# Performance work log

Measured on AMD Instinct MI355X. Metric: run time of the kernel, lower is better.

## Reference

```python
import jax, jax.numpy as jnp
import numpy as np

BETA1, BETA2, BETA3 = 0.9, 0.8, 0.9
DECAY1, INC1 = 0.05, 5.0
DECAY3, INC3 = 0.05, 5.0
LATENCY = 4.0
B_CONST = 0.15
LIF1_MIN, LIF1_MAX = 150.0, 400.0
LIF3_MIN, LIF3_MAX = 50.0, 200.0
A_P, A_M, TAU_P, TAU_M = 0.01, 0.01, 20.0, 20.0  # exponential STDP params (params1/2/3)


def stdp(dt):
    # exponential STDP curve: potentiate when post fires after pre (dt>=0), depress otherwise
    return jnp.where(dt >= 0, A_P * jnp.exp(-dt / TAU_P), -A_M * jnp.exp(dt / TAU_M))


def setup_inputs() -> dict:
    key = jax.random.key(0)
    k1, k2, k3, k4 = jax.random.split(key, 4)
    H, N, C = 8192, 4096, 128
    return {
        "image": jax.random.uniform(k1, (N,), jnp.float32),
        "W1": jax.random.uniform(k2, (H, N), jnp.float32),
        "W2": jax.random.uniform(k3, (N, H), jnp.float32),
        "W3": jax.random.uniform(k4, (C, N), jnp.float32),
        "thr1": 100.0 * jnp.ones((H,), jnp.float32),
        "thr2": 5.0 * jnp.ones((N,), jnp.float32),
        "thr3": 100.0 * jnp.ones((C,), jnp.float32),
        "time": 256,
        "pw": 8,
    }


def reference(image, W1, W2, W3, thr1, thr2, thr3, time, pw):
    N = image.shape[0]
    H = W1.shape[0]
    C = W3.shape[0]
    T = int(time)
    Tf = jnp.float32(T)

    img_t = Tf * image  # input spike times, [N]
    # rate -> pulse encoding: input_spikes[t, i] = 1 for t in [floor(img_t[i]), floor(img_t[i])+pw)
    t_axis = jnp.arange(T, dtype=jnp.float32)[:, None]          # [T,1]
    start = jnp.floor(img_t)[None, :]                            # [1,N]
    input_spikes = ((t_axis >= start) & (t_axis < start + pw)).astype(jnp.float32)  # [T,N]

    def wta(mem, th):
        # winner-take-all (snntorch inhibition=True): only argmax neuron may spike
        j = jnp.argmax(mem)
        fire = (mem[j] > th[j]).astype(mem.dtype)
        return fire * jax.nn.one_hot(j, mem.shape[0], dtype=mem.dtype)

    def step(carry, xs):
        mem1, mem2, mem3, th1, th3, r1, r2, r3, hid_act, out_act = carry
        x, t = xs
        # layer 1: Leaky LIF, inhibition, reset-to-zero
        mem1 = BETA1 * mem1 + jnp.dot(W1, x)
        spk1 = wta(mem1, th1)
        mem1 = mem1 * (1.0 - spk1)
        # layer 2: Leaky LIF, no inhibition, reset-by-subtract
        mem2 = BETA2 * mem2 + jnp.dot(W2, spk1)
        spk2 = (mem2 > thr2).astype(mem2.dtype)
        mem2 = mem2 - spk2 * thr2
        # layer 3 (clustering): Leaky LIF, inhibition, zeroed after any spike
        mem3 = BETA3 * mem3 + jnp.dot(W3, spk2)
        spk3 = wta(mem3, th3)
        mem3 = mem3 - spk3 * th3
        mem3 = jnp.where(jnp.sum(spk3) > 0, 0.0, mem3)
        # first-spike-time recon (recon stays at first nonzero spk*(t+1))
        r1 = jnp.where(r1 != 0, r1, spk1 * (t + 1.0))
        r2 = jnp.where(r2 != 0, r2, spk2 * (t + 1.0))
        r3 = jnp.where(r3 != 0, r3, spk3 * (t + 1.0))
        hid_act = hid_act + spk1
        out_act = out_act + spk2
        # adaptive thresholds: homeostatic decay + spike-triggered increase, clamped
        th1 = jnp.clip(th1 - DECAY1 + INC1 * spk1, LIF1_MIN, LIF1_MAX)
        th3 = jnp.clip(th3 - DECAY3 + INC3 * spk3, LIF3_MIN, LIF3_MAX)
        return (mem1, mem2, mem3, th1, th3, r1, r2, r3, hid_act, out_act), None

    z = jnp.zeros
    carry0 = (z(H), z(N), z(C), thr1, thr3, z(H), z(N), z(C), z(H), z(N))
    (mem1, mem2, mem3, th1, th3, r1, r2, r3, hid_act, out_act), _ = jax.lax.scan(
        step, carry0, (input_spikes, jnp.arange(T, dtype=jnp.float32)))

    # neurons that never spiked get time T
    r1 = jnp.where(r1 == 0, Tf, r1)
    r2 = jnp.where(r2 == 0, Tf, r2)
    r3 = jnp.where(r3 == 0, Tf, r3)

    # STDP weight updates (exponential), same structure as PresentImage
    hid_mask = (hid_act > 0).astype(jnp.float32)
    delta_t1 = (r1[:, None] - img_t[None, :]) * hid_mask[:, None]      # [H,N]
    W1_new = W1 + stdp(delta_t1)
    delta_t2 = r2[:, None] - r1[None, :]                                # [N,H]
    zeta = (Tf - r1) * hid_mask / Tf                                    # [H]
    rho = (r2 - LATENCY - img_t) / Tf + B_CONST                         # [N]
    W2_new = jnp.clip(W2 + stdp(delta_t2) * (rho[:, None] * zeta[None, :]), 0.0, 1.0)
    delta_t3 = r3[:, None] - r2[None, :]                                # [C,N]
    W3_new = W3 + stdp(delta_t3)

    error = (img_t - (r2 - LATENCY)) / Tf
    error_scalar = jnp.sum(jnp.square(error))
    return (error, error_scalar, r1, r2, r3, W1_new, W2_new, W3_new)
```

## Files before the change

### kernel.cpp

```cpp
#include <hip/hip_runtime.h>
#include <cstdint>
#include <cstddef>

#define Hn 8192
#define Nn 4096
#define Cn 128
#define Tt 256
#define CAP 192

typedef unsigned long long ull;

__device__ __forceinline__ float th_lazy2(float b, float lo, float hi, int nup){
    if (nup <= 0) return b;
    float a = fminf(fmaxf(__fsub_rn(b, 0.05f), lo), hi);
    if (nup == 1) return a;
    return fmaxf(__fsub_rn(a, __fmul_rn(0.05f, (float)(nup - 1))), lo);
}

__device__ __forceinline__ float clamp01(float v){
    return fminf(fmaxf(v, 0.f), 1.f);
}

template<int CTRL>
__device__ __forceinline__ int dpp_i(int x, int old){
    return __builtin_amdgcn_update_dpp(old, x, CTRL, 0xf, 0xf, false);
}
__device__ __forceinline__ float wave_max_f(float v){
    const int NEG = __float_as_int(-3.4e38f);
#define STEPM(C) { float o = __int_as_float(dpp_i<C>(__float_as_int(v), NEG)); v = fmaxf(v, o); }
    STEPM(0x111) STEPM(0x112) STEPM(0x114) STEPM(0x118) STEPM(0x142) STEPM(0x143)
#undef STEPM
    return __int_as_float(__builtin_amdgcn_readlane(__float_as_int(v), 63));
}
__device__ __forceinline__ int wave_argmax_l(float bv, int bh, float &wv, int &wh){
    float v = wave_max_f(bv);
    ull tie = __ballot(bv == v);
    int tl = __ffsll((long long)tie) - 1;
    int h = __builtin_amdgcn_readlane(bh, tl);
    if (__builtin_expect(__popcll(tie) > 1, 0)){
        ull m = tie & (tie - 1);
        while (m){
            int l2 = __ffsll((long long)m) - 1;
            int h2 = __builtin_amdgcn_readlane(bh, l2);
            if (h2 < h){ h = h2; tl = l2; }
            m &= m - 1;
        }
    }
    wv = v; wh = h; return tl;
}
__device__ __forceinline__ float rl_f(float x, int l){
    return __int_as_float(__builtin_amdgcn_readlane(__float_as_int(x), l));
}

__global__ __launch_bounds__(1024) void k_prep(const float* __restrict__ image,
        int* __restrict__ boff, int* __restrict__ sidx, unsigned* __restrict__ anyv){
    __shared__ int s_start[Nn];
    __shared__ int s_c4[4][Tt];
    __shared__ int s_boff[Tt + 1];
    int tid = threadIdx.x;
    for (int i = tid; i < Nn; i += 1024)
        s_start[i] = (int)floorf(__fmul_rn(256.f, image[i]));
    if (tid < Tt) anyv[tid] = 0u;
    __syncthreads();
    int b = tid & 255, q = tid >> 8;
    {
        int c = 0;
        for (int k = 0; k < 1024; ++k) c += (s_start[q * 1024 + k] == b) ? 1 : 0;
        s_c4[q][b] = c;
    }
    __syncthreads();
    if (tid == 0){
        int acc = 0;
        for (int bb = 0; bb < Tt; ++bb){
            s_boff[bb] = acc;
            acc += s_c4[0][bb] + s_c4[1][bb] + s_c4[2][bb] + s_c4[3][bb];
        }
        s_boff[Tt] = acc;
    }
    __syncthreads();
    if (tid <= Tt) boff[tid] = s_boff[tid];
    int p = s_boff[b];
    if (q > 0) p += s_c4[0][b];
    if (q > 1) p += s_c4[1][b];
    if (q > 2) p += s_c4[2][b];
    for (int k = 0; k < 1024; ++k){
        int i = q * 1024 + k;
        if (s_start[i] == b) sidx[p++] = i;
    }
}

__global__ __launch_bounds__(256) void k_gbuckets(const float* __restrict__ W1,
        const int* __restrict__ boff, const int* __restrict__ sidx,
        float* __restrict__ G_T){
    __shared__ float rows[4][Nn];
    int tid = threadIdx.x;
    int h0 = blockIdx.x * 4;
    for (int r = 0; r < 4; ++r){
        const float4* src = (const float4*)(W1 + (size_t)(h0 + r) * Nn);
        float4* dst = (float4*)rows[r];
        for (int j = tid; j < Nn / 4; j += 256) dst[j] = src[j];
    }
    __syncthreads();
    int t = tid;
    int b0 = boff[t], b1 = boff[t + 1];
    float s0 = 0.f, s1 = 0.f, s2 = 0.f, s3 = 0.f;
    for (int k = b0; k < b1; ++k){
        int i = sidx[k];
        s0 += rows[0][i]; s1 += rows[1][i]; s2 += rows[2][i]; s3 += rows[3][i];
    }
    G_T[(size_t)(h0 + 0) * Tt + t] = s0;
    G_T[(size_t)(h0 + 1) * Tt + t] = s1;
    G_T[(size_t)(h0 + 2) * Tt + t] = s2;
    G_T[(size_t)(h0 + 3) * Tt + t] = s3;
}

__global__ __launch_bounds__(256) void k_c1M(const float* __restrict__ G_T,
        float* __restrict__ M, float* __restrict__ r1pre, float* __restrict__ o_r1){
    __shared__ float tile[32][Tt + 1];
    __shared__ float c1s[32][Tt + 1];
    const int tid = threadIdx.x;
    const int h0 = blockIdx.x * 32;
    for (int r = 0; r < 32; ++r) tile[r][tid] = G_T[(size_t)(h0 + r) * Tt + tid];
    __syncthreads();
    {
        int hs = tid & 31, ts = tid >> 5;
        for (int tb = 0; tb < 32; ++tb){
            int t = tb * 8 + ts;
            int lo = (t - 7 < 0) ? 0 : t - 7;
            float s = 0.f;
            for (int u = lo; u <= t; ++u) s += tile[hs][u];
            c1s[hs][t] = s;
        }
    }
    __syncthreads();
    if (tid < 32){
        float m = 0.f;
        for (int t = 0; t < Tt; ++t){
            m = __fadd_rn(__fmul_rn(0.9f, m), c1s[tid][t]);
            M[(size_t)t * Hn + h0 + tid] = m;
        }
        r1pre[h0 + tid] = 0.f;
        o_r1[h0 + tid] = 256.f;
    }
}

__global__ __launch_bounds__(256) void k_sel(const float* __restrict__ M,
        float4* __restrict__ cand){
    const int t = blockIdx.x, tid = threadIdx.x;
    __shared__ float s_row[Hn];
    __shared__ unsigned s_hist[256];
    __shared__ unsigned s_suf[256];
    __shared__ unsigned s_pref;
    __shared__ int s_rank;
    __shared__ int s_cnt;
    __shared__ int s_idx[CAP + 64];
    {
        const float4* src = (const float4*)(M + (size_t)t * Hn);
        float4* d4 = (float4*)s_row;
        for (int j = tid; j < Hn / 4; j += 256) d4[j] = src[j];
    }
    if (tid == 0){ s_pref = 0u; s_rank = CAP; s_cnt = 0; }
    __syncthreads();
#pragma unroll
    for (int b = 3; b >= 0; --b){
        s_hist[tid] = 0u;
        __syncthreads();
        unsigned pref = s_pref;
        int r = s_rank;
        for (int k = 0; k < 32; ++k){
            unsigned u = __float_as_uint(s_row[tid + (k << 8)]);
            bool match = (b == 3) ? true : ((u >> ((b + 1) * 8)) == pref);
            if (match) atomicAdd(&s_hist[(u >> (b * 8)) & 255], 1u);
        }
        __syncthreads();
        s_suf[tid] = s_hist[tid];
        __syncthreads();
#pragma unroll
        for (int off = 1; off < 256; off <<= 1){
            unsigned v = (tid + off < 256) ? s_suf[tid + off] : 0u;
            __syncthreads();
            s_suf[tid] += v;
            __syncthreads();
        }
        unsigned above = s_suf[tid] - s_hist[tid];
        if ((int)above < r && r <= (int)s_suf[tid]){
            s_pref = (pref << 8) | (unsigned)tid;
            s_rank = r - (int)above;
        }
        __syncthreads();
    }
    unsigned V = s_pref;
    for (int k = 0; k < 32; ++k){
        int i = tid + (k << 8);
        unsigned u = __float_as_uint(s_row[i]);
        if (u >= V){
            int p = atomicAdd(&s_cnt, 1);
            if (p < CAP + 64) s_idx[p] = i;
        }
    }
    __syncthreads();
    int c = s_cnt;
    bool ovf = (c > CAP);
    float vV = ovf ? 3.4e38f : __uint_as_float(V);
    for (int i = tid; i < CAP; i += 256){
        float4 e;
        if (!ovf && i < c){
            int ix = s_idx[i];
            e = make_float4(s_row[ix], __int_as_float(ix | (1 << 15)), 0.f, vV);
        } else {
            e = make_float4(-1.f, 0.f, 0.f, vV);
        }
        cand[(size_t)t * CAP + i] = e;
    }
}

__global__ __launch_bounds__(256) void k_w3t(const float* __restrict__ W3,
                                             float* __restrict__ W3T){
    __shared__ float tl[64][65];
    int bx = blockIdx.x & 63, by = blockIdx.x >> 6;
    int n0 = bx * 64, c0 = by * 64;
    int tid = threadIdx.x;
    for (int e = tid; e < 64 * 64; e += 256){
        int r = e >> 6, cc = e & 63;
        tl[r][cc] = W3[(size_t)(c0 + r) * Nn + n0 + cc];
    }
    __syncthreads();
    for (int e = tid; e < 64 * 64; e += 256){
        int rn = e >> 6, cc = e & 63;
        W3T[(size_t)(n0 + rn) * Cn + c0 + cc] = tl[cc][rn];
    }
}

#define NB_W1 1024
#define NB_W2 1024

__global__ __launch_bounds__(512, 1) void k_fused(
        const float* __restrict__ M, const float4* __restrict__ cand,
        const float* __restrict__ thr1,
        const float* __restrict__ W1, const float* __restrict__ W2,
        float* __restrict__ o_W1, float* __restrict__ o_W2,
        float* __restrict__ r1pre, float* __restrict__ o_r1,
        int* __restrict__ j1s){
    __shared__ float4 s_mst[Hn];
    const int bid = blockIdx.x;
    const int tid = threadIdx.x;

    if (bid >= 1 && bid < 1 + NB_W1){
        size_t base = (size_t)(bid - 1) * 8192;
        const float4* src = (const float4*)W1;
        float4* dst = (float4*)o_W1;
        for (int i = tid; i < 8192; i += 512){
            float4 s = src[base + i];
            s.x = __fadd_rn(s.x, 0.01f); s.y = __fadd_rn(s.y, 0.01f);
            s.z = __fadd_rn(s.z, 0.01f); s.w = __fadd_rn(s.w, 0.01f);
            dst[base + i] = s;
        }
        return;
    }
    if (bid >= 1 + NB_W1){
        size_t base = (size_t)(bid - 1 - NB_W1) * 8192;
        const float4* src = (const float4*)W2;
        float4* dst = (float4*)o_W2;
        for (int i = tid; i < 8192; i += 512){
            float4 s = src[base + i];
            s.x = clamp01(s.x); s.y = clamp01(s.y);
            s.z = clamp01(s.z); s.w = clamp01(s.w);
            dst[base + i] = s;
        }
        return;
    }

    for (int h = tid; h < Hn; h += 512)
        s_mst[h] = make_float4(0.f, -1.f, thr1[h], 0.f);
    __syncthreads();
    if (tid >= 64) return;
    const int lane = tid;
    const float Lc = -0.15200309344504997f;

    float4 cA0 = cand[lane],         cA1 = cand[64 + lane],         cA2 = cand[128 + lane];
    float4 cB0 = cand[CAP + lane],   cB1 = cand[CAP + 64 + lane],   cB2 = cand[CAP + 128 + lane];
    float4 cC0 = cand[2*CAP + lane], cC1 = cand[2*CAP + 64 + lane], cC2 = cand[2*CAP + 128 + lane];
    float4 gA0 = s_mst[__float_as_int(cA0.y) & 8191];
    float4 gA1 = s_mst[__float_as_int(cA1.y) & 8191];
    float4 gA2 = s_mst[__float_as_int(cA2.y) & 8191];

    for (int t = 0; t < Tt; ++t){
        const float tf = (float)t;
        float bm = -3.4e38f; int bhh = 0x7FFFFFFF;
        float braw = 0.f, bts = 0.f, bthb = 0.f;
#define CPROC(c) { \
        int mc = __float_as_int(cA##c.y); \
        int hc = mc & 8191; \
        float dd = __fsub_rn(tf, gA##c.y); \
        float mem = __fsub_rn(cA##c.x, __fmul_rn(exp2f(__fmul_rn(dd, Lc)), gA##c.x)); \
        if (!((mc >> 15) & 1)) mem = -3.4e38f; \
        if (mem > bm || (mem == bm && hc < bhh)){ bm = mem; bhh = hc; braw = cA##c.x; bts = gA##c.y; bthb = gA##c.z; } }
        CPROC(0) CPROC(1) CPROC(2)
#undef CPROC
        const int hB0 = __float_as_int(cB0.y) & 8191;
        const int hB1 = __float_as_int(cB1.y) & 8191;
        const int hB2 = __float_as_int(cB2.y) & 8191;
        float4 gB0 = s_mst[hB0];
        float4 gB1 = s_mst[hB1];
        float4 gB2 = s_mst[hB2];
        float wv; int wh;
        int wl = wave_argmax_l(bm, bhh, wv, wh);
        float raw = rl_f(braw, wl), tsv = rl_f(bts, wl), thb = rl_f(bthb, wl);
        const float vc = cA0.w;
        int skip = 0;
        if (wv < vc){
            if (t > 0 && vc < 150.f){
                skip = 1;
            } else {
                float fv = -3.4e38f; int fh = 0x7FFFFFFF;
                float fraw = 0.f, fts = 0.f, fthb = 0.f;
                const float4* Mrow4 = (const float4*)(M + (size_t)t * Hn);
                for (int q = 0; q < 32; ++q){
                    int e = q * 64 + lane;
                    float4 mv = Mrow4[e];
                    int ib = e * 4;
                    float4 g0 = s_mst[ib+0], g1 = s_mst[ib+1], g2 = s_mst[ib+2], g3 = s_mst[ib+3];
#define FPROC(comp, gg, o2) { float x = mv.comp; float dd = __fsub_rn(tf, gg.y); \
                    float mm = __fsub_rn(x, __fmul_rn(exp2f(__fmul_rn(dd, Lc)), gg.x)); \
                    int h2 = ib + o2; \
                    if (mm > fv || (mm == fv && h2 < fh)){ fv = mm; fh = h2; fraw = x; fts = gg.y; fthb = gg.z; } }
                    FPROC(x, g0, 0) FPROC(y, g1, 1) FPROC(z, g2, 2) FPROC(w, g3, 3)
#undef FPROC
                }
                wl = wave_argmax_l(fv, fh, wv, wh);
                raw = rl_f(fraw, wl); tsv = rl_f(fts, wl); thb = rl_f(fthb, wl);
            }
        }
        int fire = 0; float thnew = 0.f;
        if (!skip){
            float te = th_lazy2(thb, 150.f, 400.f, t - (int)tsv - 1);
            if (wv > te){
                fire = 1;
                thnew = fminf(fmaxf(__fadd_rn(__fsub_rn(te, 0.05f), 5.0f), 150.f), 400.f);
            }
        }
        if (fire){
            if (lane == 0){
                j1s[t] = wh;
                if (tsv < 0.f){ o_r1[wh] = tf + 1.f; r1pre[wh] = tf + 1.f; }
                s_mst[wh] = make_float4(raw, tf, thnew, 0.f);
            }
            float4 upd = make_float4(raw, tf, thnew, 0.f);
            if (hB0 == wh) gB0 = upd;
            if (hB1 == wh) gB1 = upd;
            if (hB2 == wh) gB2 = upd;
        } else {
            if (lane == 0) j1s[t] = -1;
        }
        cA0 = cB0; cA1 = cB1; cA2 = cB2;
        cB0 = cC0; cB1 = cC1; cB2 = cC2;
        int tn = (t + 3 < Tt) ? t + 3 : Tt - 1;
        cC0 = cand[(size_t)tn * CAP + lane];
        cC1 = cand[(size_t)tn * CAP + 64 + lane];
        cC2 = cand[(size_t)tn * CAP + 128 + lane];
        gA0 = gB0; gA1 = gB1; gA2 = gB2;
    }
}

__global__ __launch_bounds__(256) void k_postmap(const int* __restrict__ j1s,
        int* __restrict__ j1slot, int* __restrict__ mh, int* __restrict__ nRout){
    __shared__ unsigned bm[256];
    __shared__ int s_j[Tt];
    __shared__ int pre[257];
    int tid = threadIdx.x;
    bm[tid] = 0u;
    s_j[tid] = j1s[tid];
    __syncthreads();
    int h = s_j[tid];
    if (h >= 0) atomicOr(&bm[h >> 5], 1u << (h & 31));
    __syncthreads();
    pre[tid + 1] = __popc(bm[tid]);
    if (tid == 0) pre[0] = 0;
    __syncthreads();
    for (int off = 1; off < 256; off <<= 1){
        int v = (tid + 1 > off) ? pre[tid + 1 - off] : 0;
        __syncthreads();
        pre[tid + 1] += v;
        __syncthreads();
    }
    {
        unsigned w = bm[tid]; int base = pre[tid];
        while (w){ int b = __ffs(w) - 1; w &= w - 1; mh[base++] = (tid << 5) | b; }
    }
    {
        int hh = s_j[tid];
        if (hh >= 0){
            int word = hh >> 5, bit = hh & 31;
            j1slot[tid] = pre[word] + __popc(bm[word] & ((1u << bit) - 1u));
        } else j1slot[tid] = -1;
    }
    if (tid == 0) *nRout = pre[256];
}

__global__ __launch_bounds__(256) void k_colg(const float* __restrict__ W2,
        const int* __restrict__ mh, const int* __restrict__ nRout,
        float* __restrict__ colv){
    int slot = blockIdx.x;
    if (slot >= *nRout) return;
    int h = mh[slot];
    int tid = threadIdx.x;
    float* dst = colv + (size_t)slot * Nn;
    for (int n = tid; n < Nn; n += 256) dst[n] = W2[(size_t)n * Hn + h];
}

__global__ __launch_bounds__(64) void k_lif2(const float* __restrict__ colv,
        const int* __restrict__ j1slot, const float* __restrict__ thr2,
        float* __restrict__ o_r2, ull* __restrict__ spkb, unsigned* __restrict__ anyv){
    __shared__ int s_j[Tt];
    int lane = threadIdx.x, blk = blockIdx.x;
    for (int i = lane; i < Tt; i += 64) s_j[i] = j1slot[i];
    __syncthreads();
    int n = blk * 64 + lane;
    float tv = thr2[n], m = 0.f, rp = 0.f;
    for (int t = 0; t < Tt; ++t){
        int s = s_j[t];
        float u = (s >= 0) ? colv[(size_t)s * Nn + n] : 0.f;
        m = __fadd_rn(__fmul_rn(0.8f, m), u);
        int f = 0;
        if (m > tv){
            m = __fsub_rn(m, tv);
            if (rp == 0.f) rp = (float)(t + 1);
            f = 1;
        }
        ull mask = __ballot(f);
        if (lane == 0){
            spkb[t * 64 + blk] = mask;
            if (mask) atomicOr(&anyv[t], 1u);
        }
    }
    o_r2[n] = (rp == 0.f) ? 256.f : rp;
}

__global__ __launch_bounds__(128, 1) void k_sim3(const ull* __restrict__ spkb,
        const unsigned* __restrict__ anyv, const float* __restrict__ W3T,
        const float* __restrict__ thr3, float* __restrict__ o_r3){
    int tid = threadIdx.x, lane = tid & 63, w = tid >> 6;
    __shared__ unsigned s_any[Tt];
    __shared__ ull s_r2[2];
    __shared__ int s_fire;
    for (int i = tid; i < Tt; i += 128) s_any[i] = anyv[i];
    float m = 0.f, th0 = thr3[tid], rp = 0.f, thv = 0.f;
    int ts = -1, zero = 1;
    __syncthreads();
    for (int t = 0; t < Tt; ++t){
        if (zero && s_any[t] == 0u) continue;
        float d = 0.f;
        if (s_any[t]){
            for (int ww = 0; ww < 64; ++ww){
                ull bits = spkb[t * 64 + ww];
                while (bits){
                    int b2 = __ffsll((long long)bits) - 1;
                    bits &= bits - 1;
                    d = __fadd_rn(d, W3T[(size_t)(ww * 64 + b2) * Cn + tid]);
                }
            }
        }
        m = __fadd_rn(__fmul_rn(0.9f, m), d);
        ull k = (((ull)__float_as_uint(m >= 0.f ? m : 0.f)) << 32) | (unsigned)(8191 - tid);
        if (!(m >= 0.f)) k = (unsigned)(8191 - tid);
#pragma unroll
        for (int off = 32; off >= 1; off >>= 1){
            ull o = __shfl_down(k, off);
            if (o > k) k = o;
        }
        if (lane == 0) s_r2[w] = k;
        __syncthreads();
        ull wk = s_r2[0] > s_r2[1] ? s_r2[0] : s_r2[1];
        int wc = 8191 - (int)(wk & 0xFFFFu);
        float wv = __uint_as_float((unsigned)(wk >> 32));
        if (tid == wc){
            float te = (ts < 0) ? th_lazy2(th0, 50.f, 200.f, t)
                                : th_lazy2(thv, 50.f, 200.f, t - ts - 1);
            int f = (wv > te) ? 1 : 0;
            s_fire = f;
            if (f){
                thv = fminf(fmaxf(__fadd_rn(__fsub_rn(te, 0.05f), 5.0f), 50.f), 200.f);
                ts = t;
                if (rp == 0.f) rp = (float)(t + 1);
            }
        }
        __syncthreads();
        if (s_fire){ m = 0.f; zero = 1; }
        else zero = 0;
        __syncthreads();
    }
    o_r3[tid] = (rp == 0.f) ? 256.f : rp;
}

__global__ __launch_bounds__(1024) void k_scalars(const float* __restrict__ image,
        const float* __restrict__ r1pre, const float* __restrict__ o_r1,
        const float* __restrict__ o_r2,
        float* __restrict__ zeta, float* __restrict__ rho,
        float* __restrict__ imgt, float* __restrict__ eiP, float* __restrict__ eiM,
        float* __restrict__ Pv, float* __restrict__ Qv,
        float* __restrict__ E2P, float* __restrict__ E2M,
        float* __restrict__ o_err, float* __restrict__ o_es){
    int tid = threadIdx.x;
    for (int h = tid; h < Hn; h += 1024){
        float r1f = o_r1[h];
        float mask = (r1pre[h] != 0.f) ? 1.f : 0.f;
        float z = __fmul_rn(__fmul_rn(__fsub_rn(256.f, r1f), mask), 0.00390625f);
        zeta[h] = z;
        Pv[h] = __expf(r1f * 0.05f) * z;
        Qv[h] = __expf(-r1f * 0.05f) * z;
    }
    float acc = 0.f;
    for (int n = tid; n < Nn; n += 1024){
        float img = __fmul_rn(256.f, image[n]);
        float r2f = o_r2[n];
        float e = __fmul_rn(__fsub_rn(img, __fsub_rn(r2f, 4.0f)), 0.00390625f);
        o_err[n] = e;
        rho[n] = __fadd_rn(__fmul_rn(__fsub_rn(__fsub_rn(r2f, 4.0f), img), 0.00390625f), 0.15f);
        imgt[n] = img;
        eiP[n] = __expf(img * 0.05f);
        eiM[n] = __expf(-img * 0.05f);
        E2P[n] = __expf(r2f * 0.05f);
        E2M[n] = __expf(-r2f * 0.05f);
        acc = __fadd_rn(acc, __fmul_rn(e, e));
    }
    __shared__ float red[16];
    for (int off = 32; off >= 1; off >>= 1) acc += __shfl_down(acc, off);
    int lane = tid & 63, w = tid >> 6;
    if (lane == 0) red[w] = acc;
    __syncthreads();
    if (tid == 0){
        float s = 0.f;
        for (int q = 0; q < 16; ++q) s += red[q];
        *o_es = s;
    }
}

__global__ __launch_bounds__(256) void k_w1fix(const float* __restrict__ W1,
        const float* __restrict__ imgt, const float* __restrict__ eiP,
        const float* __restrict__ eiM, const float* __restrict__ o_r1,
        const int* __restrict__ mh, const int* __restrict__ nRout,
        float* __restrict__ o_W1){
    int slot = blockIdx.x;
    if (slot >= *nRout) return;
    int h = mh[slot];
    int tid = threadIdx.x;
    float r1f = o_r1[h];
    float a = 0.01f * __expf(-r1f * 0.05f);
    float b = 0.01f * __expf( r1f * 0.05f);
    const float4* src = (const float4*)(W1 + (size_t)h * Nn);
    float4* dst = (float4*)(o_W1 + (size_t)h * Nn);
    const float4* ig = (const float4*)imgt;
    const float4* p4 = (const float4*)eiP;
    const float4* m4 = (const float4*)eiM;
    for (int i = tid; i < Nn / 4; i += 256){
        float4 s = src[i];
        float4 im = ig[i], pp = p4[i], mm = m4[i];
        s.x += (r1f >= im.x) ? a * pp.x : -(b * mm.x);
        s.y += (r1f >= im.y) ? a * pp.y : -(b * mm.y);
        s.z += (r1f >= im.z) ? a * pp.z : -(b * mm.z);
        s.w += (r1f >= im.w) ? a * pp.w : -(b * mm.w);
        dst[i] = s;
    }
}

__global__ __launch_bounds__(128) void k_w2fix(
        const float* __restrict__ o_r1, const float* __restrict__ Pv,
        const float* __restrict__ Qv, const float* __restrict__ o_r2,
        const float* __restrict__ rho, const int* __restrict__ mh,
        const int* __restrict__ nRout, float* __restrict__ o_W2){
    __shared__ int   s_h[Tt];
    __shared__ float s_rv[Tt], s_pp[Tt], s_qq[Tt];
    int n = blockIdx.x, tid = threadIdx.x;
    int nRv = *nRout;
    for (int s = tid; s < nRv; s += 128){
        int h = mh[s];
        s_h[s] = h; s_rv[s] = o_r1[h]; s_pp[s] = Pv[h]; s_qq[s] = Qv[h];
    }
    __syncthreads();
    float r2f = o_r2[n], rh = rho[n];
    float A = 0.01f * rh * __expf(-r2f * 0.05f);
    float B = 0.01f * rh * __expf( r2f * 0.05f);
    for (int s = tid; s < nRv; s += 128){
        size_t idx = (size_t)n * Hn + s_h[s];
        float w = o_W2[idx];
        float rv = s_rv[s];
        w = clamp01(w + ((r2f >= rv) ? A * s_pp[s] : -(B * s_qq[s])));
        o_W2[idx] = w;
    }
}

__global__ __launch_bounds__(256) void k_w3new(const float* __restrict__ W3,
        const float* __restrict__ o_r2, const float* __restrict__ E2P,
        const float* __restrict__ E2M, const float* __restrict__ o_r3,
        float* __restrict__ o_W3){
    int c = blockIdx.x, tid = threadIdx.x;
    float r3f = o_r3[c];
    float a = 0.01f * __expf(-r3f * 0.05f);
    float b = 0.01f * __expf( r3f * 0.05f);
    const float4* src = (const float4*)(W3 + (size_t)c * Nn);
    float4* dst = (float4*)(o_W3 + (size_t)c * Nn);
    const float4* r24 = (const float4*)o_r2;
    const float4* p4 = (const float4*)E2P;
    const float4* m4 = (const float4*)E2M;
    for (int i = tid; i < Nn / 4; i += 256){
        float4 s = src[i]; float4 rv = r24[i]; float4 pp = p4[i]; float4 mm = m4[i];
        s.x += (r3f >= rv.x) ? a * pp.x : -(b * mm.x);
        s.y += (r3f >= rv.y) ? a * pp.y : -(b * mm.y);
        s.z += (r3f >= rv.z) ? a * pp.z : -(b * mm.z);
        s.w += (r3f >= rv.w) ? a * pp.w : -(b * mm.w);
        dst[i] = s;
    }
}

extern "C" void kernel_launch(void* const* d_in, const int* in_sizes, int n_in,
                              void* d_out, int out_size, void* d_ws, size_t ws_size,
                              hipStream_t stream){
    const float* image = (const float*)d_in[0];
    const float* W1   = (const float*)d_in[1];
    const float* W2   = (const float*)d_in[2];
    const float* W3   = (const float*)d_in[3];
    const float* thr1 = (const float*)d_in[4];
    const float* thr2 = (const float*)d_in[5];
    const float* thr3 = (const float*)d_in[6];

    float* out  = (float*)d_out;
    float* o_err = out;
    float* o_es  = out + 4096;
    float* o_r1  = out + 4097;
    float* o_r2  = out + 12289;
    float* o_r3  = out + 16385;
    float* o_W1  = out + 16513;
    float* o_W2  = o_W1 + (size_t)Hn * Nn;
    float* o_W3  = o_W2 + (size_t)Nn * Hn;

    float* ws = (float*)d_ws;
    float* G_T   = ws;
    float* M     = G_T + (size_t)Hn * Tt;
    float* W3T   = M + (size_t)Tt * Hn;
    float* colv  = W3T + (size_t)Nn * Cn;
    float4* cand = (float4*)(colv + (size_t)256 * Nn);
    ull* spkb    = (ull*)(cand + (size_t)Tt * CAP);
    float* r1pre = (float*)(spkb + (size_t)Tt * 64);
    float* zeta  = r1pre + Hn;
    float* rho   = zeta + Hn;
    float* imgt  = rho + Nn;
    float* eiP   = imgt + Nn;
    float* eiM   = eiP + Nn;
    float* Pv    = eiM + Nn;
    float* Qv    = Pv + Hn;
    float* E2P   = Qv + Hn;
    float* E2M   = E2P + Nn;
    int* boff   = (int*)(E2M + Nn);
    int* sidx   = boff + (Tt + 1);
    int* j1s    = sidx + Nn;
    int* j1slot = j1s + Tt;
    int* mh     = j1slot + Tt;
    int* nRout  = mh + 256;
    unsigned* anyv = (unsigned*)(nRout + 1);

    k_prep<<<1, 1024, 0, stream>>>(image, boff, sidx, anyv);
    k_gbuckets<<<Hn / 4, 256, 0, stream>>>(W1, boff, sidx, G_T);
    k_c1M<<<Hn / 32, 256, 0, stream>>>(G_T, M, r1pre, o_r1);
    k_sel<<<Tt, 256, 0, stream>>>(M, cand);
    k_w3t<<<128, 256, 0, stream>>>(W3, W3T);
    k_fused<<<1 + NB_W1 + NB_W2, 512, 0, stream>>>(
        M, cand, thr1, W1, W2, o_W1, o_W2, r1pre, o_r1, j1s);
    k_postmap<<<1, 256, 0, stream>>>(j1s, j1slot, mh, nRout);
    k_colg<<<256, 256, 0, stream>>>(W2, mh, nRout, colv);
    k_lif2<<<Nn / 64, 64, 0, stream>>>(colv, j1slot, thr2, o_r2, spkb, anyv);
    k_sim3<<<1, 128, 0, stream>>>(spkb, anyv, W3T, thr3, o_r3);
    k_scalars<<<1, 1024, 0, stream>>>(image, r1pre, o_r1, o_r2, zeta, rho,
                                      imgt, eiP, eiM, Pv, Qv, E2P, E2M, o_err, o_es);
    k_w1fix<<<256, 256, 0, stream>>>(W1, imgt, eiP, eiM, o_r1, mh, nRout, o_W1);
    k_w2fix<<<Nn, 128, 0, stream>>>(o_r1, Pv, Qv, o_r2, rho, mh, nRout, o_W2);
    k_w3new<<<Cn, 256, 0, stream>>>(W3, o_r2, E2P, E2M, o_r3, o_W3);
}
```

Before: 567.2 us.

## Shrink shared memory in gbuckets and fused kernels, prefetch colv in lif2

k_gbuckets now stages 2 rows of W1 per block instead of 4. This halves its LDS footprint and doubles the grid, aiming for higher occupancy. k_fused replaces its 128 KB float4 state array with separate float, float and byte arrays and raises the launch bound to 4 blocks per CU, so the W1/W2 copy blocks can co-reside. The stored spike time is now a byte offset (t+1) decoded as ts-1, so values clamp at 255. k_lif2 software-prefetches the next timestep's colv value to hide global load latency behind the serial recurrence.

```diff
diff --git a/kernel.cpp b/kernel.cpp
--- a/kernel.cpp
+++ b/kernel.cpp
@@ -92,10 +92,10 @@
 __global__ __launch_bounds__(256) void k_gbuckets(const float* __restrict__ W1,
         const int* __restrict__ boff, const int* __restrict__ sidx,
         float* __restrict__ G_T){
-    __shared__ float rows[4][Nn];
+    __shared__ float rows[2][Nn];
     int tid = threadIdx.x;
-    int h0 = blockIdx.x * 4;
-    for (int r = 0; r < 4; ++r){
+    int h0 = blockIdx.x * 2;
+    for (int r = 0; r < 2; ++r){
         const float4* src = (const float4*)(W1 + (size_t)(h0 + r) * Nn);
         float4* dst = (float4*)rows[r];
         for (int j = tid; j < Nn / 4; j += 256) dst[j] = src[j];
@@ -103,15 +103,13 @@
     __syncthreads();
     int t = tid;
     int b0 = boff[t], b1 = boff[t + 1];
-    float s0 = 0.f, s1 = 0.f, s2 = 0.f, s3 = 0.f;
+    float s0 = 0.f, s1 = 0.f;
     for (int k = b0; k < b1; ++k){
         int i = sidx[k];
-        s0 += rows[0][i]; s1 += rows[1][i]; s2 += rows[2][i]; s3 += rows[3][i];
+        s0 += rows[0][i]; s1 += rows[1][i];
     }
     G_T[(size_t)(h0 + 0) * Tt + t] = s0;
     G_T[(size_t)(h0 + 1) * Tt + t] = s1;
-    G_T[(size_t)(h0 + 2) * Tt + t] = s2;
-    G_T[(size_t)(h0 + 3) * Tt + t] = s3;
 }
 
 __global__ __launch_bounds__(256) void k_c1M(const float* __restrict__ G_T,
@@ -234,14 +232,16 @@
 #define NB_W1 1024
 #define NB_W2 1024
 
-__global__ __launch_bounds__(512, 1) void k_fused(
+__global__ __launch_bounds__(512, 4) void k_fused(
         const float* __restrict__ M, const float4* __restrict__ cand,
         const float* __restrict__ thr1,
         const float* __restrict__ W1, const float* __restrict__ W2,
         float* __restrict__ o_W1, float* __restrict__ o_W2,
         float* __restrict__ r1pre, float* __restrict__ o_r1,
         int* __restrict__ j1s){
-    __shared__ float4 s_mst[Hn];
+    __shared__ float s_off[Hn];
+    __shared__ float s_thb[Hn];
+    __shared__ unsigned char s_ts[Hn];
     const int bid = blockIdx.x;
     const int tid = threadIdx.x;
 
@@ -270,8 +270,11 @@
         return;
     }
 
-    for (int h = tid; h < Hn; h += 512)
-        s_mst[h] = make_float4(0.f, -1.f, thr1[h], 0.f);
+    for (int h = tid; h < Hn; h += 512){
+        s_off[h] = 0.f;
+        s_thb[h] = thr1[h];
+        s_ts[h] = 0;
+    }
     __syncthreads();
     if (tid >= 64) return;
     const int lane = tid;
@@ -280,9 +283,15 @@
     float4 cA0 = cand[lane],         cA1 = cand[64 + lane],         cA2 = cand[128 + lane];
     float4 cB0 = cand[CAP + lane],   cB1 = cand[CAP + 64 + lane],   cB2 = cand[CAP + 128 + lane];
     float4 cC0 = cand[2*CAP + lane], cC1 = cand[2*CAP + 64 + lane], cC2 = cand[2*CAP + 128 + lane];
-    float4 gA0 = s_mst[__float_as_int(cA0.y) & 8191];
-    float4 gA1 = s_mst[__float_as_int(cA1.y) & 8191];
-    float4 gA2 = s_mst[__float_as_int(cA2.y) & 8191];
+    float4 gA0, gA1, gA2;
+    {
+        int h0 = __float_as_int(cA0.y) & 8191;
+        int h1 = __float_as_int(cA1.y) & 8191;
+        int h2 = __float_as_int(cA2.y) & 8191;
+        gA0 = make_float4(s_off[h0], (float)s_ts[h0] - 1.f, s_thb[h0], 0.f);
+        gA1 = make_float4(s_off[h1], (float)s_ts[h1] - 1.f, s_thb[h1], 0.f);
+        gA2 = make_float4(s_off[h2], (float)s_ts[h2] - 1.f, s_thb[h2], 0.f);
+    }
 
     for (int t = 0; t < Tt; ++t){
         const float tf = (float)t;
@@ -300,9 +309,9 @@
         const int hB0 = __float_as_int(cB0.y) & 8191;
         const int hB1 = __float_as_int(cB1.y) & 8191;
         const int hB2 = __float_as_int(cB2.y) & 8191;
-        float4 gB0 = s_mst[hB0];
-        float4 gB1 = s_mst[hB1];
-        float4 gB2 = s_mst[hB2];
+        float4 gB0 = make_float4(s_off[hB0], (float)s_ts[hB0] - 1.f, s_thb[hB0], 0.f);
+        float4 gB1 = make_float4(s_off[hB1], (float)s_ts[hB1] - 1.f, s_thb[hB1], 0.f);
+        float4 gB2 = make_float4(s_off[hB2], (float)s_ts[hB2] - 1.f, s_thb[hB2], 0.f);
         float wv; int wh;
         int wl = wave_argmax_l(bm, bhh, wv, wh);
         float raw = rl_f(braw, wl), tsv = rl_f(bts, wl), thb = rl_f(bthb, wl);
@@ -319,12 +328,12 @@
                     int e = q * 64 + lane;
                     float4 mv = Mrow4[e];
                     int ib = e * 4;
-                    float4 g0 = s_mst[ib+0], g1 = s_mst[ib+1], g2 = s_mst[ib+2], g3 = s_mst[ib+3];
-#define FPROC(comp, gg, o2) { float x = mv.comp; float dd = __fsub_rn(tf, gg.y); \
-                    float mm = __fsub_rn(x, __fmul_rn(exp2f(__fmul_rn(dd, Lc)), gg.x)); \
-                    int h2 = ib + o2; \
-                    if (mm > fv || (mm == fv && h2 < fh)){ fv = mm; fh = h2; fraw = x; fts = gg.y; fthb = gg.z; } }
-                    FPROC(x, g0, 0) FPROC(y, g1, 1) FPROC(z, g2, 2) FPROC(w, g3, 3)
+#define FPROC(comp, o2) { float x = mv.comp; int h2 = ib + o2; \
+                    float gts = (float)s_ts[h2] - 1.f; \
+                    float dd = __fsub_rn(tf, gts); \
+                    float mm = __fsub_rn(x, __fmul_rn(exp2f(__fmul_rn(dd, Lc)), s_off[h2])); \
+                    if (mm > fv || (mm == fv && h2 < fh)){ fv = mm; fh = h2; fraw = x; fts = gts; fthb = s_thb[h2]; } }
+                    FPROC(x, 0) FPROC(y, 1) FPROC(z, 2) FPROC(w, 3)
 #undef FPROC
                 }
                 wl = wave_argmax_l(fv, fh, wv, wh);
@@ -343,7 +352,9 @@
             if (lane == 0){
                 j1s[t] = wh;
                 if (tsv < 0.f){ o_r1[wh] = tf + 1.f; r1pre[wh] = tf + 1.f; }
-                s_mst[wh] = make_float4(raw, tf, thnew, 0.f);
+                s_off[wh] = raw;
+                s_ts[wh] = (unsigned char)((t + 1 < 256) ? (t + 1) : 255);
+                s_thb[wh] = thnew;
             }
             float4 upd = make_float4(raw, tf, thnew, 0.f);
             if (hB0 == wh) gB0 = upd;
@@ -417,10 +428,15 @@
     __syncthreads();
     int n = blk * 64 + lane;
     float tv = thr2[n], m = 0.f, rp = 0.f;
+    int s0v = s_j[0];
+    float u0 = (s0v >= 0) ? colv[(size_t)s0v * Nn + n] : 0.f;
     for (int t = 0; t < Tt; ++t){
-        int s = s_j[t];
-        float u = (s >= 0) ? colv[(size_t)s * Nn + n] : 0.f;
-        m = __fadd_rn(__fmul_rn(0.8f, m), u);
+        float u1 = 0.f;
+        if (t + 1 < Tt){
+            int s1v = s_j[t + 1];
+            if (s1v >= 0) u1 = colv[(size_t)s1v * Nn + n];
+        }
+        m = __fadd_rn(__fmul_rn(0.8f, m), u0);
         int f = 0;
         if (m > tv){
             m = __fsub_rn(m, tv);
@@ -432,6 +448,7 @@
             spkb[t * 64 + blk] = mask;
             if (mask) atomicOr(&anyv[t], 1u);
         }
+        u0 = u1;
     }
     o_r2[n] = (rp == 0.f) ? 256.f : rp;
 }
@@ -659,7 +676,7 @@
     unsigned* anyv = (unsigned*)(nRout + 1);
 
     k_prep<<<1, 1024, 0, stream>>>(image, boff, sidx, anyv);
-    k_gbuckets<<<Hn / 4, 256, 0, stream>>>(W1, boff, sidx, G_T);
+    k_gbuckets<<<Hn / 2, 256, 0, stream>>>(W1, boff, sidx, G_T);
     k_c1M<<<Hn / 32, 256, 0, stream>>>(G_T, M, r1pre, o_r1);
     k_sel<<<Tt, 256, 0, stream>>>(M, cand);
     k_w3t<<<128, 256, 0, stream>>>(W3, W3T);
```

After: 563.5 us. About the same (-0.7%).
